# Kernel tuning notes

Hardware: AMD Instinct MI355X
Metric: run time of the kernel (lower is better)

The kernel has to match this reference:

```python
import jax, jax.numpy as jnp
import numpy as np

MAX_EXP_ARG = 80.0
EPS = 1e-6
SMALL = 1e-4

D_MODEL = 1024
D_STATE = 16


def setup_inputs() -> dict:
    key = jax.random.key(0)
    k1, k2, k3, k4 = jax.random.split(key, 4)
    b, l, d, n = 2, 2048, D_MODEL, D_STATE
    x = jax.random.normal(k1, (b, l, d), dtype=jnp.float32)
    B = jax.random.normal(k2, (b, l, n), dtype=jnp.float32)
    C = jax.random.normal(k3, (b, l, n), dtype=jnp.float32)
    delta = jax.random.normal(k4, (b, l, d), dtype=jnp.float32)
    # parameters per SSMKernel.__init__
    A_log = jnp.broadcast_to(jnp.log(jnp.arange(1, n + 1, dtype=jnp.float32)), (d, n))
    D_param = jnp.ones((d,), dtype=jnp.float32)
    return {"x": x, "B": B, "C": C, "delta": delta, "A_log": A_log, "D_param": D_param}


def _safe_exp(v):
    return jnp.exp(jnp.minimum(v, MAX_EXP_ARG))


def _ssm_forward(x, B, C, delta, A_log, D_param):
    b, l, d = x.shape
    n = A_log.shape[-1]
    A = -jnp.exp(A_log)                                  # (d, n), negative
    dt = jax.nn.softplus(delta)[..., None]               # (b, l, d, 1)
    delta_A = dt * A[None, None]                         # (b, l, d, n)
    A_bar = _safe_exp(delta_A)
    abs_dA = jnp.abs(delta_A)
    taylor = 1.0 + delta_A / 2.0 + (delta_A * delta_A) / 6.0
    exact = jnp.where(abs_dA > EPS,
                      (A_bar - 1.0) / (delta_A + EPS * jnp.sign(delta_A)),
                      jnp.ones_like(delta_A))
    scaling = jnp.where(abs_dA < SMALL, taylor, exact)
    B_bar = dt * scaling * B[:, :, None, :]              # (b, l, d, n)
    Bx = B_bar * x[..., None]                            # (b, l, d, n)

    # sequential selective scan: h_t = A_bar_t * h_{t-1} + Bx_t ; y_t = C_t . h_t
    def step(h, inp):
        a_t, bx_t, c_t = inp                              # (b,d,n), (b,d,n), (b,n)
        h = a_t * h + bx_t
        y_t = jnp.einsum('bdn,bn->bd', h, c_t)
        return h, y_t

    h0 = jnp.zeros((b, d, n), dtype=x.dtype)
    scan_in = (jnp.swapaxes(A_bar, 0, 1), jnp.swapaxes(Bx, 0, 1), jnp.swapaxes(C, 0, 1))
    _, ys = jax.lax.scan(step, h0, scan_in)              # ys: (l, b, d)
    y = jnp.swapaxes(ys, 0, 1)                           # (b, l, d)
    return y + D_param[None, None, :] * x


def reference(x, B, C, delta, A_log, D_param):
    return _ssm_forward(x, B, C, delta, A_log, D_param)
```

## Files before the change

kernel.cpp:

```cpp
#include <hip/hip_runtime.h>
#include <cstdint>
#include <cstddef>

#define BB 2
#define LL 2048
#define DD 1024
#define NN 16
#define NP (NN / 2)
#define LC 32
#define CH (LL / LC)
#define XT (DD / 256)

typedef float v2f __attribute__((ext_vector_type(2)));

__device__ __forceinline__ v2f vfma(v2f a, v2f b, v2f c) {
#if __has_builtin(__builtin_elementwise_fma)
    return __builtin_elementwise_fma(a, b, c);
#else
    v2f r; r.x = fmaf(a.x, b.x, c.x); r.y = fmaf(a.y, b.y, c.y); return r;
#endif
}

__device__ __constant__ float INV_NP1[NN] = {
    1.0f/1, 1.0f/2, 1.0f/3, 1.0f/4, 1.0f/5, 1.0f/6, 1.0f/7, 1.0f/8,
    1.0f/9, 1.0f/10, 1.0f/11, 1.0f/12, 1.0f/13, 1.0f/14, 1.0f/15, 1.0f/16 };

__device__ __forceinline__ float decay_r(float delta) {
    return __builtin_amdgcn_rcpf(1.0f + __expf(delta));
}

__global__ __launch_bounds__(256, 2) void ssm_pass1(
    const float* __restrict__ xg, const float* __restrict__ Bg,
    const float* __restrict__ dg,
    float* __restrict__ Pc, float* __restrict__ Sc)
{
    const int tid = threadIdx.x;
    const int d   = blockIdx.x * 256 + tid;
    const int cc  = blockIdx.y;
    const int bb  = blockIdx.z;
    const int t0  = cc * LC;

    __shared__ float sB[LC * NN];
    {
        const float* bp = Bg + ((size_t)bb * LL + t0) * NN;
        sB[tid]       = bp[tid]       * INV_NP1[tid & (NN - 1)];
        sB[tid + 256] = bp[tid + 256] * INV_NP1[tid & (NN - 1)];
    }
    __syncthreads();

    float dtv[LC], xvv[LC];
    {
        const float* dp = dg + ((size_t)bb * LL + t0) * DD + d;
        const float* xp = xg + ((size_t)bb * LL + t0) * DD + d;
#pragma unroll
        for (int tl = 0; tl < LC; ++tl) { dtv[tl] = dp[(size_t)tl * DD]; xvv[tl] = xp[(size_t)tl * DD]; }
    }

    v2f S[NP];
#pragma unroll
    for (int p = 0; p < NP; ++p) S[p] = (v2f){0.0f, 0.0f};
    float P = 1.0f;

    const v2f* sBv = (const v2f*)sB;
#pragma unroll
    for (int tl = 0; tl < LC; ++tl) {
        float r  = decay_r(dtv[tl]);
        float xv = xvv[tl];
        P *= r;
        float r2 = r * r;
        const v2f xa2 = (v2f){-xv, -xv};
        const v2f r22 = (v2f){r2, r2};
        v2f a2 = (v2f){r, r2};
#pragma unroll
        for (int p = 0; p < NP; ++p) {
            v2f u = sBv[tl * NP + p] * xa2;
            S[p] = vfma(a2, S[p] + u, -u);
            a2 = a2 * r22;
        }
    }

    Pc[((size_t)bb * CH + cc) * DD + d] = P;
    {
        float* sp = Sc + (((size_t)bb * CH + cc) * NN) * DD + d;
#pragma unroll
        for (int p = 0; p < NP; ++p) {
            sp[(size_t)(2*p)   * DD] = S[p].x;
            sp[(size_t)(2*p+1) * DD] = S[p].y;
        }
    }
}

__global__ __launch_bounds__(256) void ssm_pass2(
    const float* __restrict__ Pc, float* __restrict__ Sc)
{
    const int flat = blockIdx.x * 256 + threadIdx.x;
    const int d  = flat & (DD - 1);
    const int n  = (flat >> 10) & (NN - 1);
    const int bb = flat >> 14;
    const int e  = n + 1;

    const size_t stride = (size_t)NN * DD;
    const size_t base   = ((size_t)bb * CH * NN + n) * DD + d;
    const size_t tb     = (size_t)bb * CH * DD + d;

    float h = 0.0f;
    for (int cb = 0; cb < CH; cb += 16) {
        float Pv[16], Sv[16];
#pragma unroll
        for (int j = 0; j < 16; ++j) {
            Pv[j] = Pc[tb + (size_t)(cb + j) * DD];
            Sv[j] = Sc[base + (size_t)(cb + j) * stride];
        }
        float Dv[16];
#pragma unroll
        for (int j = 0; j < 16; ++j) {
            float p1 = Pv[j], p2 = p1 * p1, p4 = p2 * p2, p8 = p4 * p4;
            float dcy = 1.0f;
            if (e & 1)  dcy *= p1;
            if (e & 2)  dcy *= p2;
            if (e & 4)  dcy *= p4;
            if (e & 8)  dcy *= p8;
            if (e & 16) dcy *= p8 * p8;
            Dv[j] = dcy;
        }
#pragma unroll
        for (int j = 0; j < 16; ++j) {
            Sc[base + (size_t)(cb + j) * stride] = h;
            h = fmaf(Dv[j], h, Sv[j]);
        }
    }
}

__global__ __launch_bounds__(256, 2) void ssm_pass3(
    const float* __restrict__ xg, const float* __restrict__ Bg,
    const float* __restrict__ Cg, const float* __restrict__ dg,
    const float* __restrict__ Dg,
    const float* __restrict__ HS, float* __restrict__ out)
{
    const int tid = threadIdx.x;
    const int d   = blockIdx.x * 256 + tid;
    const int cc  = blockIdx.y;
    const int bb  = blockIdx.z;
    const int t0  = cc * LC;

    __shared__ float sB[LC * NN];
    __shared__ float sC[LC * NN];
    {
        const float* bp = Bg + ((size_t)bb * LL + t0) * NN;
        const float* cp = Cg + ((size_t)bb * LL + t0) * NN;
        sB[tid]       = bp[tid]       * INV_NP1[tid & (NN - 1)];
        sB[tid + 256] = bp[tid + 256] * INV_NP1[tid & (NN - 1)];
        sC[tid]       = cp[tid];
        sC[tid + 256] = cp[tid + 256];
    }
    __syncthreads();

    v2f h[NP];
    {
        const float* hp = HS + (((size_t)bb * CH + cc) * NN) * DD + d;
#pragma unroll
        for (int p = 0; p < NP; ++p) {
            h[p].x = hp[(size_t)(2*p)   * DD];
            h[p].y = hp[(size_t)(2*p+1) * DD];
        }
    }
    const float Dd = Dg[d];

    float dtv[LC], xvv[LC];
    {
        const float* dp = dg + ((size_t)bb * LL + t0) * DD + d;
        const float* xp = xg + ((size_t)bb * LL + t0) * DD + d;
#pragma unroll
        for (int tl = 0; tl < LC; ++tl) { dtv[tl] = dp[(size_t)tl * DD]; xvv[tl] = xp[(size_t)tl * DD]; }
    }

    float* op = out + ((size_t)bb * LL + t0) * DD + d;
    const v2f* sBv = (const v2f*)sB;
    const v2f* sCv = (const v2f*)sC;

#pragma unroll
    for (int tl = 0; tl < LC; ++tl) {
        float r  = decay_r(dtv[tl]);
        float xv = xvv[tl];
        float r2 = r * r;
        const v2f xa2 = (v2f){-xv, -xv};
        const v2f r22 = (v2f){r2, r2};
        v2f a2 = (v2f){r, r2};
        v2f y0 = (v2f){0.f, 0.f}, y1 = (v2f){0.f, 0.f};
        v2f y2 = (v2f){0.f, 0.f}, y3 = (v2f){0.f, 0.f};
#pragma unroll
        for (int p = 0; p < NP; ++p) {
            v2f u = sBv[tl * NP + p] * xa2;
            h[p] = vfma(a2, h[p] + u, -u);
            v2f cv = sCv[tl * NP + p];
            if ((p & 3) == 0)      y0 = vfma(h[p], cv, y0);
            else if ((p & 3) == 1) y1 = vfma(h[p], cv, y1);
            else if ((p & 3) == 2) y2 = vfma(h[p], cv, y2);
            else                   y3 = vfma(h[p], cv, y3);
            a2 = a2 * r22;
        }
        v2f ys = (y0 + y1) + (y2 + y3);
        op[(size_t)tl * DD] = (ys.x + ys.y) + Dd * xv;
    }
}

extern "C" void kernel_launch(void* const* d_in, const int* in_sizes, int n_in,
                              void* d_out, int out_size, void* d_ws, size_t ws_size,
                              hipStream_t stream) {
    const float* xg = (const float*)d_in[0];
    const float* Bg = (const float*)d_in[1];
    const float* Cg = (const float*)d_in[2];
    const float* dg = (const float*)d_in[3];
    const float* Dg = (const float*)d_in[5];
    float* out = (float*)d_out;

    float* Pc = (float*)d_ws;
    float* Sc = Pc + (size_t)BB * CH * DD;

    ssm_pass1<<<dim3(XT, CH, BB), 256, 0, stream>>>(xg, Bg, dg, Pc, Sc);
    ssm_pass2<<<dim3((BB * DD * NN) / 256, 1, 1), 256, 0, stream>>>(Pc, Sc);
    ssm_pass3<<<dim3(XT, CH, BB), 256, 0, stream>>>(xg, Bg, Cg, dg, Dg, Sc, out);
}
```

Baseline: 112.8 us.

## Stage x/delta via float4 into LDS, shrink blocks, split chunk scan into segments

Pass1 and pass3 now use 128-thread blocks and load x and delta with float4 into shared memory, where decay_r is precomputed. Each thread then reads its per-step values from LDS instead of keeping them in 32-element register arrays. Pass2 splits the 64-chunk carry scan into 4 segments per (b,d,n), combined through shared memory, giving 4x more threads and a shorter serial chain. The cost is extra LDS traffic and syncs, plus more blocks with less work each.

After: 113.9 us. Within noise of the previous version (+0.9%).

```diff
diff --git a/kernel.cpp b/kernel.cpp
--- a/kernel.cpp
+++ b/kernel.cpp
@@ -9,7 +9,10 @@
 #define NP (NN / 2)
 #define LC 32
 #define CH (LL / LC)
-#define XT (DD / 256)
+#define DT 128
+#define XT2 (DD / DT)
+#define SEGS 4
+#define SCH (CH / SEGS)
 
 typedef float v2f __attribute__((ext_vector_type(2)));
 
@@ -29,32 +32,49 @@
     return __builtin_amdgcn_rcpf(1.0f + __expf(delta));
 }
 
-__global__ __launch_bounds__(256, 2) void ssm_pass1(
+__global__ __launch_bounds__(128, 2) void ssm_pass1(
     const float* __restrict__ xg, const float* __restrict__ Bg,
     const float* __restrict__ dg,
     float* __restrict__ Pc, float* __restrict__ Sc)
 {
     const int tid = threadIdx.x;
-    const int d   = blockIdx.x * 256 + tid;
+    const int dt0 = blockIdx.x * DT;
+    const int d   = dt0 + tid;
     const int cc  = blockIdx.y;
     const int bb  = blockIdx.z;
     const int t0  = cc * LC;
 
+    __shared__ float sR[LC * DT];
+    __shared__ float sX[LC * DT];
     __shared__ float sB[LC * NN];
+
     {
         const float* bp = Bg + ((size_t)bb * LL + t0) * NN;
-        sB[tid]       = bp[tid]       * INV_NP1[tid & (NN - 1)];
-        sB[tid + 256] = bp[tid + 256] * INV_NP1[tid & (NN - 1)];
-    }
-    __syncthreads();
-
-    float dtv[LC], xvv[LC];
-    {
-        const float* dp = dg + ((size_t)bb * LL + t0) * DD + d;
-        const float* xp = xg + ((size_t)bb * LL + t0) * DD + d;
-#pragma unroll
-        for (int tl = 0; tl < LC; ++tl) { dtv[tl] = dp[(size_t)tl * DD]; xvv[tl] = xp[(size_t)tl * DD]; }
-    }
+        const float inv = INV_NP1[tid & (NN - 1)];
+#pragma unroll
+        for (int k = 0; k < 4; ++k) sB[tid + k * DT] = bp[tid + k * DT] * inv;
+    }
+    {
+        const float* xrow = xg + ((size_t)bb * LL + t0) * DD + dt0;
+        const float* drow = dg + ((size_t)bb * LL + t0) * DD + dt0;
+        float4 xv[8], dv[8];
+#pragma unroll
+        for (int k = 0; k < 8; ++k) {
+            const int f = k * DT + tid, t = f >> 5, c4 = f & 31;
+            xv[k] = ((const float4*)(xrow + (size_t)t * DD))[c4];
+            dv[k] = ((const float4*)(drow + (size_t)t * DD))[c4];
+        }
+#pragma unroll
+        for (int k = 0; k < 8; ++k) {
+            const int f = k * DT + tid;
+            ((float4*)sX)[f] = xv[k];
+            float4 rv;
+            rv.x = decay_r(dv[k].x); rv.y = decay_r(dv[k].y);
+            rv.z = decay_r(dv[k].z); rv.w = decay_r(dv[k].w);
+            ((float4*)sR)[f] = rv;
+        }
+    }
+    __syncthreads();
 
     v2f S[NP];
 #pragma unroll
@@ -64,10 +84,10 @@
     const v2f* sBv = (const v2f*)sB;
 #pragma unroll
     for (int tl = 0; tl < LC; ++tl) {
-        float r  = decay_r(dtv[tl]);
-        float xv = xvv[tl];
+        const float r  = sR[tl * DT + tid];
+        const float xv = sX[tl * DT + tid];
         P *= r;
-        float r2 = r * r;
+        const float r2 = r * r;
         const v2f xa2 = (v2f){-xv, -xv};
         const v2f r22 = (v2f){r2, r2};
         v2f a2 = (v2f){r, r2};
@@ -93,86 +113,127 @@
 __global__ __launch_bounds__(256) void ssm_pass2(
     const float* __restrict__ Pc, float* __restrict__ Sc)
 {
-    const int flat = blockIdx.x * 256 + threadIdx.x;
-    const int d  = flat & (DD - 1);
-    const int n  = (flat >> 10) & (NN - 1);
-    const int bb = flat >> 14;
-    const int e  = n + 1;
+    const int tid = threadIdx.x;
+    const int tup = tid & 63;
+    const int seg = tid >> 6;
+    const int g   = blockIdx.x * 64 + tup;
+    const int d   = g & (DD - 1);
+    const int n   = (g >> 10) & (NN - 1);
+    const int b   = g >> 14;
+    const int e   = n + 1;
+    const int cc0 = seg * SCH;
+
+    __shared__ float s2[64 * 9];
 
     const size_t stride = (size_t)NN * DD;
-    const size_t base   = ((size_t)bb * CH * NN + n) * DD + d;
-    const size_t tb     = (size_t)bb * CH * DD + d;
-
-    float h = 0.0f;
-    for (int cb = 0; cb < CH; cb += 16) {
-        float Pv[16], Sv[16];
-#pragma unroll
-        for (int j = 0; j < 16; ++j) {
-            Pv[j] = Pc[tb + (size_t)(cb + j) * DD];
-            Sv[j] = Sc[base + (size_t)(cb + j) * stride];
-        }
-        float Dv[16];
-#pragma unroll
-        for (int j = 0; j < 16; ++j) {
-            float p1 = Pv[j], p2 = p1 * p1, p4 = p2 * p2, p8 = p4 * p4;
-            float dcy = 1.0f;
-            if (e & 1)  dcy *= p1;
-            if (e & 2)  dcy *= p2;
-            if (e & 4)  dcy *= p4;
-            if (e & 8)  dcy *= p8;
-            if (e & 16) dcy *= p8 * p8;
-            Dv[j] = dcy;
-        }
-#pragma unroll
-        for (int j = 0; j < 16; ++j) {
-            Sc[base + (size_t)(cb + j) * stride] = h;
-            h = fmaf(Dv[j], h, Sv[j]);
-        }
-    }
-}
-
-__global__ __launch_bounds__(256, 2) void ssm_pass3(
+    const size_t sbase  = ((size_t)b * CH * NN + n) * DD + d + (size_t)cc0 * stride;
+    const size_t pbase  = ((size_t)b * CH + cc0) * DD + d;
+
+    float Pv[SCH], Sv[SCH];
+#pragma unroll
+    for (int j = 0; j < SCH; ++j) {
+        Pv[j] = Pc[pbase + (size_t)j * DD];
+        Sv[j] = Sc[sbase + (size_t)j * stride];
+    }
+    float Dv[SCH];
+#pragma unroll
+    for (int j = 0; j < SCH; ++j) {
+        float p1 = Pv[j], p2 = p1 * p1, p4 = p2 * p2, p8 = p4 * p4;
+        float dcy = 1.0f;
+        if (e & 1)  dcy *= p1;
+        if (e & 2)  dcy *= p2;
+        if (e & 4)  dcy *= p4;
+        if (e & 8)  dcy *= p8;
+        if (e & 16) dcy *= p8 * p8;
+        Dv[j] = dcy;
+    }
+    float A = 0.0f, Dt = 1.0f;
+#pragma unroll
+    for (int j = 0; j < SCH; ++j) { A = fmaf(Dv[j], A, Sv[j]); Dt *= Dv[j]; }
+    s2[tup * 9 + seg * 2]     = Dt;
+    s2[tup * 9 + seg * 2 + 1] = A;
+    __syncthreads();
+    if (seg == 0) {
+        const float a0  = s2[tup*9 + 1];
+        const float g1  = s2[tup*9 + 2], a1  = s2[tup*9 + 3];
+        const float g2  = s2[tup*9 + 4], a2s = s2[tup*9 + 5];
+        const float h1 = a0;
+        const float h2 = fmaf(g1, h1, a1);
+        const float h3 = fmaf(g2, h2, a2s);
+        s2[tup*9 + 1] = 0.0f;
+        s2[tup*9 + 3] = h1;
+        s2[tup*9 + 5] = h2;
+        s2[tup*9 + 7] = h3;
+    }
+    __syncthreads();
+    float h = s2[tup * 9 + seg * 2 + 1];
+#pragma unroll
+    for (int j = 0; j < SCH; ++j) {
+        Sc[sbase + (size_t)j * stride] = h;
+        h = fmaf(Dv[j], h, Sv[j]);
+    }
+}
+
+__global__ __launch_bounds__(128, 2) void ssm_pass3(
     const float* __restrict__ xg, const float* __restrict__ Bg,
     const float* __restrict__ Cg, const float* __restrict__ dg,
     const float* __restrict__ Dg,
     const float* __restrict__ HS, float* __restrict__ out)
 {
     const int tid = threadIdx.x;
-    const int d   = blockIdx.x * 256 + tid;
+    const int dt0 = blockIdx.x * DT;
+    const int d   = dt0 + tid;
     const int cc  = blockIdx.y;
     const int bb  = blockIdx.z;
     const int t0  = cc * LC;
 
+    __shared__ float sR[LC * DT];
+    __shared__ float sX[LC * DT];
     __shared__ float sB[LC * NN];
     __shared__ float sC[LC * NN];
+
+    v2f h[NP];
+    {
+        const float* hp = HS + (((size_t)bb * CH + cc) * NN) * DD + d;
+#pragma unroll
+        for (int p = 0; p < NP; ++p) {
+            h[p].x = hp[(size_t)(2*p)   * DD];
+            h[p].y = hp[(size_t)(2*p+1) * DD];
+        }
+    }
+    const float Dd = Dg[d];
+
     {
         const float* bp = Bg + ((size_t)bb * LL + t0) * NN;
         const float* cp = Cg + ((size_t)bb * LL + t0) * NN;
-        sB[tid]       = bp[tid]       * INV_NP1[tid & (NN - 1)];
-        sB[tid + 256] = bp[tid + 256] * INV_NP1[tid & (NN - 1)];
-        sC[tid]       = cp[tid];
-        sC[tid + 256] = cp[tid + 256];
-    }
-    __syncthreads();
-
-    v2f h[NP];
-    {
-        const float* hp = HS + (((size_t)bb * CH + cc) * NN) * DD + d;
-#pragma unroll
-        for (int p = 0; p < NP; ++p) {
-            h[p].x = hp[(size_t)(2*p)   * DD];
-            h[p].y = hp[(size_t)(2*p+1) * DD];
-        }
-    }
-    const float Dd = Dg[d];
-
-    float dtv[LC], xvv[LC];
-    {
-        const float* dp = dg + ((size_t)bb * LL + t0) * DD + d;
-        const float* xp = xg + ((size_t)bb * LL + t0) * DD + d;
-#pragma unroll
-        for (int tl = 0; tl < LC; ++tl) { dtv[tl] = dp[(size_t)tl * DD]; xvv[tl] = xp[(size_t)tl * DD]; }
-    }
+        const float inv = INV_NP1[tid & (NN - 1)];
+#pragma unroll
+        for (int k = 0; k < 4; ++k) {
+            sB[tid + k * DT] = bp[tid + k * DT] * inv;
+            sC[tid + k * DT] = cp[tid + k * DT];
+        }
+    }
+    {
+        const float* xrow = xg + ((size_t)bb * LL + t0) * DD + dt0;
+        const float* drow = dg + ((size_t)bb * LL + t0) * DD + dt0;
+        float4 xv[8], dv[8];
+#pragma unroll
+        for (int k = 0; k < 8; ++k) {
+            const int f = k * DT + tid, t = f >> 5, c4 = f & 31;
+            xv[k] = ((const float4*)(xrow + (size_t)t * DD))[c4];
+            dv[k] = ((const float4*)(drow + (size_t)t * DD))[c4];
+        }
+#pragma unroll
+        for (int k = 0; k < 8; ++k) {
+            const int f = k * DT + tid;
+            ((float4*)sX)[f] = xv[k];
+            float4 rv;
+            rv.x = decay_r(dv[k].x); rv.y = decay_r(dv[k].y);
+            rv.z = decay_r(dv[k].z); rv.w = decay_r(dv[k].w);
+            ((float4*)sR)[f] = rv;
+        }
+    }
+    __syncthreads();
 
     float* op = out + ((size_t)bb * LL + t0) * DD + d;
     const v2f* sBv = (const v2f*)sB;
@@ -180,9 +241,9 @@
 
 #pragma unroll
     for (int tl = 0; tl < LC; ++tl) {
-        float r  = decay_r(dtv[tl]);
-        float xv = xvv[tl];
-        float r2 = r * r;
+        const float r  = sR[tl * DT + tid];
+        const float xv = sX[tl * DT + tid];
+        const float r2 = r * r;
         const v2f xa2 = (v2f){-xv, -xv};
         const v2f r22 = (v2f){r2, r2};
         v2f a2 = (v2f){r, r2};
@@ -217,7 +278,7 @@
     float* Pc = (float*)d_ws;
     float* Sc = Pc + (size_t)BB * CH * DD;
 
-    ssm_pass1<<<dim3(XT, CH, BB), 256, 0, stream>>>(xg, Bg, dg, Pc, Sc);
-    ssm_pass2<<<dim3((BB * DD * NN) / 256, 1, 1), 256, 0, stream>>>(Pc, Sc);
-    ssm_pass3<<<dim3(XT, CH, BB), 256, 0, stream>>>(xg, Bg, Cg, dg, Dg, Sc, out);
-}
+    ssm_pass1<<<dim3(XT2, CH, BB), 128, 0, stream>>>(xg, Bg, dg, Pc, Sc);
+    ssm_pass2<<<dim3((BB * DD * NN * SEGS) / 256, 1, 1), 256, 0, stream>>>(Pc, Sc);
+    ssm_pass3<<<dim3(XT2, CH, BB), 128, 0, stream>>>(xg, Bg, Cg, dg, Dg, Sc, out);
+}
```
